# Performance work log

Measured on AMD Instinct MI355X. Metric: run time of the kernel, lower is better.

The kernel has to match this reference:

```python
import jax, jax.numpy as jnp
import numpy as np
import math

N_HEADS = 32
N_KV_HEADS = 8
HEAD_DIM = 64
ROPE_BASE = 10000.0


def _rope_cos_sin(L, dtype):
    # inv_freq: [head_dim/2]
    inv_freq = 1.0 / (ROPE_BASE ** (jnp.arange(0, HEAD_DIM, 2, dtype=jnp.float32) / HEAD_DIM))
    t = jnp.arange(L, dtype=jnp.float32)
    freqs = jnp.outer(t, inv_freq)            # [L, head_dim/2]
    emb = jnp.concatenate([freqs, freqs], -1)  # [L, head_dim]
    return jnp.cos(emb).astype(dtype), jnp.sin(emb).astype(dtype)


def _rotate_half(x):
    x1, x2 = jnp.split(x, 2, axis=-1)
    return jnp.concatenate([-x2, x1], axis=-1)


def setup_inputs() -> dict:
    key = jax.random.key(0)
    ks = jax.random.split(key, 5)
    B, L, D = 2, 2048, 2048
    s = 0.02
    return {
        "x": jax.random.normal(ks[0], (B, L, D), jnp.float32),
        "Wq": jax.random.normal(ks[1], (D, N_HEADS * HEAD_DIM), jnp.float32) * s,
        "Wk": jax.random.normal(ks[2], (D, N_KV_HEADS * HEAD_DIM), jnp.float32) * s,
        "Wv": jax.random.normal(ks[3], (D, N_KV_HEADS * HEAD_DIM), jnp.float32) * s,
        "Wo": jax.random.normal(ks[4], (N_HEADS * HEAD_DIM, D), jnp.float32) * s,
    }


def reference(x, Wq, Wk, Wv, Wo):
    B, L, D = x.shape
    G = N_HEADS // N_KV_HEADS
    # QKV projections -> [B, H, L, hd]
    q = (x @ Wq).reshape(B, L, N_HEADS, HEAD_DIM).transpose(0, 2, 1, 3)
    k = (x @ Wk).reshape(B, L, N_KV_HEADS, HEAD_DIM).transpose(0, 2, 1, 3)
    v = (x @ Wv).reshape(B, L, N_KV_HEADS, HEAD_DIM).transpose(0, 2, 1, 3)
    # RoPE
    cos, sin = _rope_cos_sin(L, x.dtype)  # [L, hd]
    cos = cos[None, None]
    sin = sin[None, None]
    q = q * cos + _rotate_half(q) * sin
    k = k * cos + _rotate_half(k) * sin
    # GQA expand kv heads (repeat_interleave along head dim)
    k = jnp.repeat(k, G, axis=1)
    v = jnp.repeat(v, G, axis=1)
    # Causal SDPA
    scale = 1.0 / math.sqrt(HEAD_DIM)
    scores = jnp.einsum('bhqd,bhkd->bhqk', q, k) * scale  # [B,H,L,L]
    causal = jnp.tril(jnp.ones((L, L), bool))
    scores = jnp.where(causal[None, None], scores, jnp.finfo(scores.dtype).min)
    probs = jax.nn.softmax(scores, axis=-1)
    out = jnp.einsum('bhqk,bhkd->bhqd', probs, v)  # [B,H,L,hd]
    out = out.transpose(0, 2, 1, 3).reshape(B, L, N_HEADS * HEAD_DIM)
    return out @ Wo
```

## Files before the change

kernel.cpp:

```cpp
#include <hip/hip_runtime.h>
#include <hip/hip_bf16.h>
#include <stdint.h>

typedef __bf16 bf16_t;
typedef bf16_t bf16x2 __attribute__((ext_vector_type(2)));
typedef bf16_t bf16x4 __attribute__((ext_vector_type(4)));
typedef bf16_t bf16x8 __attribute__((ext_vector_type(8)));
typedef float f32x4 __attribute__((ext_vector_type(4)));
typedef float f32x16 __attribute__((ext_vector_type(16)));

#define NH 32
#define NKV 8
#define HD 64
#define LSEQ 2048
#define DMODEL 2048
#define BATCH 2

#define QSCALE 0.18033688011112042f
#define FIXED_M 12.0f

__device__ __forceinline__ void gl_lds16(const void* g, void* l) {
  __builtin_amdgcn_global_load_lds(
      (__attribute__((address_space(1))) char*)(uintptr_t)g,
      (__attribute__((address_space(3))) char*)(uintptr_t)l, 16, 0, 0);
}

__device__ __forceinline__ unsigned pack2(float a, float b) {
  bf16x2 t;
  t[0] = (bf16_t)a;
  t[1] = (bf16_t)b;
  return __builtin_bit_cast(unsigned, t);
}


__global__ void cvt_x(const float4* __restrict__ s, bf16x4* __restrict__ d, int n4) {
  int i = blockIdx.x * blockDim.x + threadIdx.x;
  if (i >= n4) return;
  float4 v = s[i];
  bf16x4 o;
  o[0] = (bf16_t)v.x; o[1] = (bf16_t)v.y; o[2] = (bf16_t)v.z; o[3] = (bf16_t)v.w;
  d[i] = o;
}

__global__ void transpose_w(const float* __restrict__ W, bf16_t* __restrict__ WT,
                            int K, int N) {
  __shared__ float tile[32][33];
  int nb = blockIdx.x * 32, kb = blockIdx.y * 32;
  int tx = threadIdx.x, ty = threadIdx.y;
#pragma unroll
  for (int i = 0; i < 32; i += 8)
    tile[ty + i][tx] = W[(size_t)(kb + ty + i) * N + nb + tx];
  __syncthreads();
#pragma unroll
  for (int i = 0; i < 32; i += 8)
    WT[(size_t)(nb + ty + i) * K + kb + tx] = (bf16_t)tile[tx][ty + i];
}

__global__ void rope_table(float* __restrict__ cosT, float* __restrict__ sinT) {
  int t = blockIdx.x * blockDim.x + threadIdx.x;
  int l = t >> 5, i = t & 31;
  float inv = powf(10000.0f, -(float)i / 32.0f);
  float ang = (float)l * inv;
  float s, c;
  sincosf(ang, &s, &c);
  cosT[t] = c;
  sinT[t] = s;
}

template <int EPI, int NREP>
__global__ __launch_bounds__(512, 1) void gemm256(
    const bf16_t* __restrict__ A, const bf16_t* __restrict__ BT,
    float* __restrict__ Cf, bf16_t* __restrict__ Qo, bf16_t* __restrict__ Ko,
    bf16_t* __restrict__ Vo, int M, int N, int K,
    const float* __restrict__ cosT, const float* __restrict__ sinT, int nx) {
  constexpr int BN = NREP * 64;
  __shared__ bf16_t Al[2][4 * 4096];
  __shared__ bf16_t Bl[2][NREP * 4096];
  const int tid = threadIdx.x, lane = tid & 63, w = tid >> 6;
  const int wm = w >> 2, wn = w & 3;
  const int r15 = lane & 15, g = lane >> 4;
  const int nwg = (int)gridDim.x;
  const int sid = ((int)blockIdx.x & 7) * (nwg >> 3) + ((int)blockIdx.x >> 3);
  const int m0 = (sid / nx) * 256, n0 = (sid % nx) * BN;

  f32x4 acc[8][NREP] = {};

  const int NT = K >> 6;
  const int NI = NT >> 1;

  auto stage_q = [&](bf16_t* dst, const bf16_t* src, int row0, int kt) {
    const int r = tid >> 3;
    const int sc = (((tid & 7) ^ (r & 7)) << 3);
    gl_lds16(src + (size_t)(row0 + r) * K + (kt << 6) + sc, dst + tid * 8);
  };
  auto stage_step = [&](int d, int kt, int s) {
    kt = kt < NT ? kt : NT - 1;
    if (NREP == 4) {
      if (s == 0) { stage_q(&Bl[d][0], BT, n0, kt); stage_q(&Bl[d][4096], BT, n0 + 64, kt); }
      else if (s == 1) { stage_q(&Bl[d][8192], BT, n0 + 128, kt); stage_q(&Bl[d][12288], BT, n0 + 192, kt); }
      else if (s == 2) { stage_q(&Al[d][0], A, m0, kt); stage_q(&Al[d][8192], A, m0 + 128, kt); }
      else { stage_q(&Al[d][4096], A, m0 + 64, kt); stage_q(&Al[d][12288], A, m0 + 192, kt); }
    } else {
      if (s == 0) { stage_q(&Bl[d][0], BT, n0, kt); stage_q(&Bl[d][4096], BT, n0 + 64, kt); }
      else if (s == 1) { stage_q(&Al[d][0], A, m0, kt); stage_q(&Al[d][8192], A, m0 + 128, kt); }
      else if (s == 2) { stage_q(&Al[d][4096], A, m0 + 64, kt); stage_q(&Al[d][12288], A, m0 + 192, kt); }
    }
  };
  auto lda = [&](int d, int mi, int kk) -> bf16x8 {
    const int ar = (wm << 7) + (mi << 4) + r15;
    return *(const bf16x8*)((const char*)&Al[d][(ar >> 6) << 12] +
                            (ar & 63) * 128 + ((((kk << 2) + g) ^ (ar & 7)) << 4));
  };
  auto ldb = [&](int d, int ni, int kk) -> bf16x8 {
    const int br = wn * (NREP << 4) + (ni << 4) + r15;
    return *(const bf16x8*)((const char*)&Bl[d][(br >> 6) << 12] +
                            (br & 63) * 128 + ((((kk << 2) + g) ^ (br & 7)) << 4));
  };

  stage_step(0, 0, 0);
  stage_step(0, 0, 1);
  stage_step(0, 0, 2);
  stage_step(0, 0, 3);

  for (int i = 0; i < NI; ++i) {
#pragma unroll
    for (int hf = 0; hf < 2; ++hf) {
      const int dC = hf;
      const int dS = hf ^ 1;
      const int ktS = (i << 1) + 1 + hf;
      bf16x8 bf0[NREP][2];
#pragma unroll
      for (int q = 0; q < 4; ++q) {
        stage_step(dS, ktS, q);
        if (q == 0) asm volatile("s_waitcnt vmcnt(4)" ::: "memory");
        if (q == 2) asm volatile("s_waitcnt vmcnt(6)" ::: "memory");
        __builtin_amdgcn_s_barrier();
        asm volatile("" ::: "memory");
        if (q == 0) {
#pragma unroll
          for (int ni = 0; ni < NREP; ++ni)
#pragma unroll
            for (int kk = 0; kk < 2; ++kk) bf0[ni][kk] = ldb(dC, ni, kk);
        }
        bf16x8 af[2][2];
#pragma unroll
        for (int t2 = 0; t2 < 2; ++t2)
#pragma unroll
          for (int kk = 0; kk < 2; ++kk) af[t2][kk] = lda(dC, 2 * q + t2, kk);
        __builtin_amdgcn_s_setprio(1);
#pragma unroll
        for (int t2 = 0; t2 < 2; ++t2)
#pragma unroll
          for (int ni = 0; ni < NREP; ++ni)
#pragma unroll
            for (int kk = 0; kk < 2; ++kk)
              acc[2 * q + t2][ni] = __builtin_amdgcn_mfma_f32_16x16x32_bf16(
                  af[t2][kk], bf0[ni][kk], acc[2 * q + t2][ni], 0, 0, 0);
        __builtin_amdgcn_s_setprio(0);
        asm volatile("" ::: "memory");
        __builtin_amdgcn_s_barrier();
      }
    }
  }
  asm volatile("s_waitcnt vmcnt(0)" ::: "memory");

  if constexpr (EPI == 0) {
#pragma unroll
    for (int mi = 0; mi < 8; ++mi) {
      const int row = m0 + wm * 128 + mi * 16 + g * 4;
#pragma unroll
      for (int ni = 0; ni < NREP; ++ni) {
        const int col = n0 + wn * (NREP * 16) + ni * 16 + r15;
#pragma unroll
        for (int r = 0; r < 4; ++r)
          Cf[(size_t)(row + r) * N + col] = acc[mi][ni][r];
      }
    }
  } else {
    const int colbase = n0 + wn * 64;
    auto rope_store = [&](bf16_t* C, int NHT, int colrel, float sc) {
#pragma unroll
      for (int mi = 0; mi < 8; ++mi)
#pragma unroll
        for (int r = 0; r < 4; ++r) {
          const int rowg = m0 + wm * 128 + mi * 16 + g * 4 + r;
          const int bb = rowg >> 11, ls = rowg & (LSEQ - 1);
#pragma unroll
          for (int ni = 0; ni < 2; ++ni) {
            const int col = colrel + ni * 16 + r15;
            const int hh = col >> 6, d = col & 63;
            const float c = cosT[ls * 32 + d], s = sinT[ls * 32 + d];
            const float v0 = acc[mi][ni][r], v1 = acc[mi][ni + 2][r];
            bf16_t* dst = C + (((size_t)bb * NHT + hh) * LSEQ + ls) * HD + d;
            dst[0] = (bf16_t)((v0 * c - v1 * s) * sc);
            dst[32] = (bf16_t)((v1 * c + v0 * s) * sc);
          }
        }
    };
    if (n0 < 2048) {
      rope_store(Qo, NH, colbase, QSCALE);
    } else if (n0 < 2560) {
      rope_store(Ko, NKV, colbase - 2048, 1.0f);
    } else {
#pragma unroll
      for (int mi = 0; mi < 8; ++mi)
#pragma unroll
        for (int r = 0; r < 4; ++r) {
          const int rowg = m0 + wm * 128 + mi * 16 + g * 4 + r;
          const int bb = rowg >> 11, ls = rowg & (LSEQ - 1);
#pragma unroll
          for (int ni = 0; ni < 4; ++ni) {
            const int col = colbase - 2560 + ni * 16 + r15;
            const int hh = col >> 6, d = col & 63;
            Vo[(((size_t)bb * NKV + hh) * HD + d) * LSEQ + ls] =
                (bf16_t)acc[mi][ni][r];
          }
        }
    }
  }
}

__global__ __launch_bounds__(512, 4) void attn_fwd(
    const bf16_t* __restrict__ Q, const bf16_t* __restrict__ Kh,
    const bf16_t* __restrict__ VTh, bf16_t* __restrict__ AO) {
  __shared__ bf16_t Kl[2][64 * 64];
  __shared__ bf16_t Vl[2][64 * 64];
  const int tid = threadIdx.x, lane = tid & 63, w = tid >> 6;
  const int col = lane & 31, hi = lane >> 5;
  const int hk = (int)blockIdx.x & 7, b = (int)blockIdx.x >> 3;
  const int a = (int)blockIdx.y & 15, k = (int)blockIdx.y >> 4;
  const int qt = k ? 31 - a : a;
  const int h = hk * 4 + (w & 3);
  const int qoff = (w >> 2) * 32;

  const bf16_t* Qb =
      Q + (((size_t)b * NH + h) * LSEQ + (size_t)qt * 64 + qoff) * HD;
  const bf16_t* Kb = Kh + ((size_t)b * NKV + hk) * LSEQ * HD;
  const bf16_t* Vb = VTh + ((size_t)b * NKV + hk) * HD * LSEQ;

  const int nt = qt + 1;

  bf16x8 ones8;
#pragma unroll
  for (int j = 0; j < 8; ++j) ones8[j] = (bf16_t)1.0f;

  auto stage = [&](int buf, int kt) {
    const int row = tid >> 3, cc = tid & 7;
    const int scol = (cc ^ (row & 7)) * 16;
    gl_lds16((const char*)Kb + (size_t)(kt * 64 + row) * 128 + scol,
             (char*)&Kl[buf][0] + tid * 16);
    gl_lds16((const char*)Vb + (size_t)row * 4096 + (size_t)kt * 128 + scol,
             (char*)&Vl[buf][0] + tid * 16);
  };

  bf16x8 qf[4];
#pragma unroll
  for (int kc = 0; kc < 4; ++kc)
    qf[kc] = *(const bf16x8*)&Qb[(size_t)col * HD + kc * 16 + hi * 8];

  f32x16 o[2] = {};
  f32x16 osum = {};

  int cur = 0;
  stage(cur, 0);
  __syncthreads();
  for (int kt = 0; kt < nt; ++kt) {
    if (kt + 1 < nt) stage(cur ^ 1, kt + 1);
    const bool diag = (kt == nt - 1);
    const char* Kcur = (const char*)&Kl[cur][0];
    const char* Vcur = (const char*)&Vl[cur][0];

    f32x16 sfrag[2] = {};
#pragma unroll
    for (int kvs = 0; kvs < 2; ++kvs) {
      if (diag && kvs * 32 > 31 + qoff) {
#pragma unroll
        for (int r = 0; r < 16; ++r) sfrag[kvs][r] = -1e30f;
        continue;
      }
      bf16x8 ak[4];
#pragma unroll
      for (int kc = 0; kc < 4; ++kc) {
        const int row = kvs * 32 + col;
        const int slot = ((kc * 2 + hi) ^ (row & 7)) * 16;
        ak[kc] = *(const bf16x8*)(Kcur + row * 128 + slot);
      }
#pragma unroll
      for (int kc = 0; kc < 4; ++kc)
        sfrag[kvs] = __builtin_amdgcn_mfma_f32_32x32x16_bf16(
            ak[kc], qf[kc], sfrag[kvs], 0, 0, 0);
    }

    if (diag) {
#pragma unroll
      for (int kvs = 0; kvs < 2; ++kvs)
#pragma unroll
        for (int r = 0; r < 16; ++r) {
          const int kvl = kvs * 32 + (r & 3) + 8 * (r >> 2) + 4 * hi;
          if (kvl > col + qoff) sfrag[kvs][r] = -1e30f;
        }
    }

    bf16x8 pf[4];
#pragma unroll
    for (int kvs = 0; kvs < 2; ++kvs)
#pragma unroll
      for (int c1 = 0; c1 < 2; ++c1) {
        float pv[8];
#pragma unroll
        for (int j = 0; j < 8; ++j)
          pv[j] = __builtin_amdgcn_exp2f(sfrag[kvs][c1 * 8 + j] - FIXED_M);
        const unsigned a01 = pack2(pv[0], pv[1]), a23 = pack2(pv[2], pv[3]);
        const unsigned b01 = pack2(pv[4], pv[5]), b23 = pack2(pv[6], pv[7]);
        const unsigned s01 = __shfl_xor(hi ? a01 : b01, 32);
        const unsigned s23 = __shfl_xor(hi ? a23 : b23, 32);
        union { unsigned u[4]; bf16x8 v; } t;
        t.u[0] = hi ? s01 : a01;
        t.u[1] = hi ? s23 : a23;
        t.u[2] = hi ? b01 : s01;
        t.u[3] = hi ? b23 : s23;
        pf[kvs * 2 + c1] = t.v;
      }

#pragma unroll
    for (int ds = 0; ds < 2; ++ds) {
      bf16x8 av[4];
#pragma unroll
      for (int kc2 = 0; kc2 < 4; ++kc2) {
        const int row = ds * 32 + col;
        const int slot = ((kc2 * 2 + hi) ^ (row & 7)) * 16;
        av[kc2] = *(const bf16x8*)(Vcur + row * 128 + slot);
      }
#pragma unroll
      for (int kc2 = 0; kc2 < 4; ++kc2) {
        if (diag && kc2 * 16 > 31 + qoff) continue;
        o[ds] = __builtin_amdgcn_mfma_f32_32x32x16_bf16(
            av[kc2], pf[kc2], o[ds], 0, 0, 0);
      }
    }
#pragma unroll
    for (int kc2 = 0; kc2 < 4; ++kc2) {
      if (diag && kc2 * 16 > 31 + qoff) continue;
      osum = __builtin_amdgcn_mfma_f32_32x32x16_bf16(
          ones8, pf[kc2], osum, 0, 0, 0);
    }

    __syncthreads();
    cur ^= 1;
  }

  const float inv = 1.0f / osum[0];
  const int q = qt * 64 + qoff + col;
#pragma unroll
  for (int ds = 0; ds < 2; ++ds)
#pragma unroll
    for (int g4 = 0; g4 < 4; ++g4) {
      bf16x4 o4;
#pragma unroll
      for (int j = 0; j < 4; ++j) o4[j] = (bf16_t)(o[ds][g4 * 4 + j] * inv);
      const int d = ds * 32 + 8 * g4 + 4 * hi;
      *(bf16x4*)&AO[((size_t)b * LSEQ + q) * DMODEL + h * HD + d] = o4;
    }
}


extern "C" void kernel_launch(void* const* d_in, const int* in_sizes, int n_in,
                              void* d_out, int out_size, void* d_ws, size_t ws_size,
                              hipStream_t stream) {
  const float* x = (const float*)d_in[0];
  const float* Wq = (const float*)d_in[1];
  const float* Wk = (const float*)d_in[2];
  const float* Wv = (const float*)d_in[3];
  const float* Wo = (const float*)d_in[4];
  char* ws = (char*)d_ws;
  size_t off = 0;
  auto alloc = [&](size_t bytes) {
    char* p = ws + off;
    off += (bytes + 255) & ~(size_t)255;
    return p;
  };
  bf16_t* xb = (bf16_t*)alloc((size_t)BATCH * LSEQ * DMODEL * 2);
  bf16_t* wqkvT = (bf16_t*)alloc((size_t)3072 * DMODEL * 2);
  bf16_t* wot = (bf16_t*)alloc((size_t)DMODEL * DMODEL * 2);
  float* cosT = (float*)alloc((size_t)LSEQ * 32 * 4);
  float* sinT = (float*)alloc((size_t)LSEQ * 32 * 4);
  bf16_t* Qh = (bf16_t*)alloc((size_t)BATCH * NH * LSEQ * HD * 2);
  bf16_t* Kh = (bf16_t*)alloc((size_t)BATCH * NKV * LSEQ * HD * 2);
  bf16_t* VTh = (bf16_t*)alloc((size_t)BATCH * NKV * HD * LSEQ * 2);
  bf16_t* AO = (bf16_t*)alloc((size_t)BATCH * LSEQ * NH * HD * 2);
  (void)ws_size; (void)in_sizes; (void)n_in; (void)out_size;

  const int M = BATCH * LSEQ;

  cvt_x<<<(M * DMODEL / 4 + 255) / 256, 256, 0, stream>>>(
      (const float4*)x, (bf16x4*)xb, M * DMODEL / 4);
  transpose_w<<<dim3(64, 64), dim3(32, 8), 0, stream>>>(Wq, wqkvT, 2048, 2048);
  transpose_w<<<dim3(16, 64), dim3(32, 8), 0, stream>>>(
      Wk, wqkvT + (size_t)2048 * 2048, 2048, 512);
  transpose_w<<<dim3(16, 64), dim3(32, 8), 0, stream>>>(
      Wv, wqkvT + (size_t)2560 * 2048, 2048, 512);
  transpose_w<<<dim3(64, 64), dim3(32, 8), 0, stream>>>(Wo, wot, 2048, 2048);
  rope_table<<<LSEQ * 32 / 256, 256, 0, stream>>>(cosT, sinT);

  gemm256<3, 4><<<192, 512, 0, stream>>>(
      xb, wqkvT, nullptr, Qh, Kh, VTh, M, 3072, 2048, cosT, sinT, 12);

  attn_fwd<<<dim3(16, 32), 512, 0, stream>>>(Qh, Kh, VTh, AO);

  gemm256<0, 2><<<256, 512, 0, stream>>>(
      AO, wot, (float*)d_out, nullptr, nullptr, nullptr, M, 2048, 2048,
      nullptr, nullptr, 16);
}
```

Baseline: 173.8 us.

## Replace pipelined 256x256 QKV GEMM with simple 128x128 tile kernel

The QKV projection moves from a 256x256-tile, 512-thread, double-buffered LDS-pipelined GEMM (192 blocks) to a new 128x128-tile, 256-thread kernel with a single LDS buffer and plain syncthreads (768 blocks, up to 3 per CU). The aim is a better fit of work to the CU count and more occupancy to hide latency. In exchange it gives up the explicit load/compute overlap and accepts more global traffic from the smaller tiles. The output-projection GEMM is kept, with its unused epilogue parameters removed.

Result: no change. 173.3 us (-0.3%).

```diff
diff --git a/kernel.cpp b/kernel.cpp
--- a/kernel.cpp
+++ b/kernel.cpp
@@ -67,110 +67,64 @@
   sinT[t] = s;
 }
 
-template <int EPI, int NREP>
-__global__ __launch_bounds__(512, 1) void gemm256(
+template <int EPI>
+__global__ __launch_bounds__(256, 3) void gemm128(
     const bf16_t* __restrict__ A, const bf16_t* __restrict__ BT,
     float* __restrict__ Cf, bf16_t* __restrict__ Qo, bf16_t* __restrict__ Ko,
     bf16_t* __restrict__ Vo, int M, int N, int K,
     const float* __restrict__ cosT, const float* __restrict__ sinT, int nx) {
-  constexpr int BN = NREP * 64;
-  __shared__ bf16_t Al[2][4 * 4096];
-  __shared__ bf16_t Bl[2][NREP * 4096];
+  __shared__ bf16_t Al[128 * 64];
+  __shared__ bf16_t Bl[128 * 64];
   const int tid = threadIdx.x, lane = tid & 63, w = tid >> 6;
-  const int wm = w >> 2, wn = w & 3;
+  const int wm = w >> 1, wn = w & 1;
   const int r15 = lane & 15, g = lane >> 4;
   const int nwg = (int)gridDim.x;
   const int sid = ((int)blockIdx.x & 7) * (nwg >> 3) + ((int)blockIdx.x >> 3);
-  const int m0 = (sid / nx) * 256, n0 = (sid % nx) * BN;
-
-  f32x4 acc[8][NREP] = {};
-
-  const int NT = K >> 6;
-  const int NI = NT >> 1;
-
-  auto stage_q = [&](bf16_t* dst, const bf16_t* src, int row0, int kt) {
-    const int r = tid >> 3;
-    const int sc = (((tid & 7) ^ (r & 7)) << 3);
-    gl_lds16(src + (size_t)(row0 + r) * K + (kt << 6) + sc, dst + tid * 8);
-  };
-  auto stage_step = [&](int d, int kt, int s) {
-    kt = kt < NT ? kt : NT - 1;
-    if (NREP == 4) {
-      if (s == 0) { stage_q(&Bl[d][0], BT, n0, kt); stage_q(&Bl[d][4096], BT, n0 + 64, kt); }
-      else if (s == 1) { stage_q(&Bl[d][8192], BT, n0 + 128, kt); stage_q(&Bl[d][12288], BT, n0 + 192, kt); }
-      else if (s == 2) { stage_q(&Al[d][0], A, m0, kt); stage_q(&Al[d][8192], A, m0 + 128, kt); }
-      else { stage_q(&Al[d][4096], A, m0 + 64, kt); stage_q(&Al[d][12288], A, m0 + 192, kt); }
-    } else {
-      if (s == 0) { stage_q(&Bl[d][0], BT, n0, kt); stage_q(&Bl[d][4096], BT, n0 + 64, kt); }
-      else if (s == 1) { stage_q(&Al[d][0], A, m0, kt); stage_q(&Al[d][8192], A, m0 + 128, kt); }
-      else if (s == 2) { stage_q(&Al[d][4096], A, m0 + 64, kt); stage_q(&Al[d][12288], A, m0 + 192, kt); }
-    }
-  };
-  auto lda = [&](int d, int mi, int kk) -> bf16x8 {
-    const int ar = (wm << 7) + (mi << 4) + r15;
-    return *(const bf16x8*)((const char*)&Al[d][(ar >> 6) << 12] +
-                            (ar & 63) * 128 + ((((kk << 2) + g) ^ (ar & 7)) << 4));
-  };
-  auto ldb = [&](int d, int ni, int kk) -> bf16x8 {
-    const int br = wn * (NREP << 4) + (ni << 4) + r15;
-    return *(const bf16x8*)((const char*)&Bl[d][(br >> 6) << 12] +
-                            (br & 63) * 128 + ((((kk << 2) + g) ^ (br & 7)) << 4));
-  };
-
-  stage_step(0, 0, 0);
-  stage_step(0, 0, 1);
-  stage_step(0, 0, 2);
-  stage_step(0, 0, 3);
-
-  for (int i = 0; i < NI; ++i) {
-#pragma unroll
-    for (int hf = 0; hf < 2; ++hf) {
-      const int dC = hf;
-      const int dS = hf ^ 1;
-      const int ktS = (i << 1) + 1 + hf;
-      bf16x8 bf0[NREP][2];
-#pragma unroll
-      for (int q = 0; q < 4; ++q) {
-        stage_step(dS, ktS, q);
-        if (q == 0) asm volatile("s_waitcnt vmcnt(4)" ::: "memory");
-        if (q == 2) asm volatile("s_waitcnt vmcnt(6)" ::: "memory");
-        __builtin_amdgcn_s_barrier();
-        asm volatile("" ::: "memory");
-        if (q == 0) {
-#pragma unroll
-          for (int ni = 0; ni < NREP; ++ni)
-#pragma unroll
-            for (int kk = 0; kk < 2; ++kk) bf0[ni][kk] = ldb(dC, ni, kk);
-        }
-        bf16x8 af[2][2];
-#pragma unroll
-        for (int t2 = 0; t2 < 2; ++t2)
-#pragma unroll
-          for (int kk = 0; kk < 2; ++kk) af[t2][kk] = lda(dC, 2 * q + t2, kk);
-        __builtin_amdgcn_s_setprio(1);
-#pragma unroll
-        for (int t2 = 0; t2 < 2; ++t2)
-#pragma unroll
-          for (int ni = 0; ni < NREP; ++ni)
-#pragma unroll
-            for (int kk = 0; kk < 2; ++kk)
-              acc[2 * q + t2][ni] = __builtin_amdgcn_mfma_f32_16x16x32_bf16(
-                  af[t2][kk], bf0[ni][kk], acc[2 * q + t2][ni], 0, 0, 0);
-        __builtin_amdgcn_s_setprio(0);
-        asm volatile("" ::: "memory");
-        __builtin_amdgcn_s_barrier();
-      }
-    }
+  const int m0 = (sid / nx) * 128, n0 = (sid % nx) * 128;
+  f32x4 acc[4][4] = {};
+
+  for (int kt = 0; kt < K; kt += 64) {
+#pragma unroll
+    for (int i = 0; i < 4; ++i) {
+      const int c = i * 256 + tid;
+      const int row = c >> 3, cc = c & 7;
+      const int sc = (cc ^ (row & 7)) * 8;
+      gl_lds16(A + (size_t)(m0 + row) * K + kt + sc, Al + c * 8);
+      gl_lds16(BT + (size_t)(n0 + row) * K + kt + sc, Bl + c * 8);
+    }
+    __syncthreads();
+#pragma unroll
+    for (int kk = 0; kk < 2; ++kk) {
+      bf16x8 af[4], bfr[4];
+#pragma unroll
+      for (int mi = 0; mi < 4; ++mi) {
+        const int r = wm * 64 + mi * 16 + r15;
+        af[mi] = *(const bf16x8*)((const char*)Al + r * 128 +
+                                  (((kk * 4 + g) ^ (r & 7)) << 4));
+      }
+#pragma unroll
+      for (int ni = 0; ni < 4; ++ni) {
+        const int r = wn * 64 + ni * 16 + r15;
+        bfr[ni] = *(const bf16x8*)((const char*)Bl + r * 128 +
+                                   (((kk * 4 + g) ^ (r & 7)) << 4));
+      }
+#pragma unroll
+      for (int mi = 0; mi < 4; ++mi)
+#pragma unroll
+        for (int ni = 0; ni < 4; ++ni)
+          acc[mi][ni] = __builtin_amdgcn_mfma_f32_16x16x32_bf16(
+              af[mi], bfr[ni], acc[mi][ni], 0, 0, 0);
+    }
+    __syncthreads();
   }
-  asm volatile("s_waitcnt vmcnt(0)" ::: "memory");
 
   if constexpr (EPI == 0) {
 #pragma unroll
-    for (int mi = 0; mi < 8; ++mi) {
-      const int row = m0 + wm * 128 + mi * 16 + g * 4;
-#pragma unroll
-      for (int ni = 0; ni < NREP; ++ni) {
-        const int col = n0 + wn * (NREP * 16) + ni * 16 + r15;
+    for (int mi = 0; mi < 4; ++mi) {
+      const int row = m0 + wm * 64 + mi * 16 + g * 4;
+#pragma unroll
+      for (int ni = 0; ni < 4; ++ni) {
+        const int col = n0 + wn * 64 + ni * 16 + r15;
 #pragma unroll
         for (int r = 0; r < 4; ++r)
           Cf[(size_t)(row + r) * N + col] = acc[mi][ni][r];
@@ -180,10 +134,10 @@
     const int colbase = n0 + wn * 64;
     auto rope_store = [&](bf16_t* C, int NHT, int colrel, float sc) {
 #pragma unroll
-      for (int mi = 0; mi < 8; ++mi)
+      for (int mi = 0; mi < 4; ++mi)
 #pragma unroll
         for (int r = 0; r < 4; ++r) {
-          const int rowg = m0 + wm * 128 + mi * 16 + g * 4 + r;
+          const int rowg = m0 + wm * 64 + mi * 16 + g * 4 + r;
           const int bb = rowg >> 11, ls = rowg & (LSEQ - 1);
 #pragma unroll
           for (int ni = 0; ni < 2; ++ni) {
@@ -203,10 +157,10 @@
       rope_store(Ko, NKV, colbase - 2048, 1.0f);
     } else {
 #pragma unroll
-      for (int mi = 0; mi < 8; ++mi)
+      for (int mi = 0; mi < 4; ++mi)
 #pragma unroll
         for (int r = 0; r < 4; ++r) {
-          const int rowg = m0 + wm * 128 + mi * 16 + g * 4 + r;
+          const int rowg = m0 + wm * 64 + mi * 16 + g * 4 + r;
           const int bb = rowg >> 11, ls = rowg & (LSEQ - 1);
 #pragma unroll
           for (int ni = 0; ni < 4; ++ni) {
@@ -216,6 +170,106 @@
                 (bf16_t)acc[mi][ni][r];
           }
         }
+    }
+  }
+}
+
+template <int EPI, int NREP>
+__global__ __launch_bounds__(512, 1) void gemm256(
+    const bf16_t* __restrict__ A, const bf16_t* __restrict__ BT,
+    float* __restrict__ Cf, int M, int N, int K, int nx) {
+  __shared__ bf16_t Al[2][4 * 4096];
+  __shared__ bf16_t Bl[2][NREP * 4096];
+  const int tid = threadIdx.x, lane = tid & 63, w = tid >> 6;
+  const int wm = w >> 2, wn = w & 3;
+  const int r15 = lane & 15, g = lane >> 4;
+  const int nwg = (int)gridDim.x;
+  const int sid = ((int)blockIdx.x & 7) * (nwg >> 3) + ((int)blockIdx.x >> 3);
+  const int m0 = (sid / nx) * 256, n0 = (sid % nx) * (NREP * 64);
+
+  f32x4 acc[8][NREP] = {};
+
+  const int NT = K >> 6;
+  const int NI = NT >> 1;
+
+  auto stage_q = [&](bf16_t* dst, const bf16_t* src, int row0, int kt) {
+    const int r = tid >> 3;
+    const int sc = (((tid & 7) ^ (r & 7)) << 3);
+    gl_lds16(src + (size_t)(row0 + r) * K + (kt << 6) + sc, dst + tid * 8);
+  };
+  auto stage_step = [&](int d, int kt, int s) {
+    kt = kt < NT ? kt : NT - 1;
+    if (s == 0) { stage_q(&Bl[d][0], BT, n0, kt); stage_q(&Bl[d][4096], BT, n0 + 64, kt); }
+    else if (s == 1) { stage_q(&Al[d][0], A, m0, kt); stage_q(&Al[d][8192], A, m0 + 128, kt); }
+    else if (s == 2) { stage_q(&Al[d][4096], A, m0 + 64, kt); stage_q(&Al[d][12288], A, m0 + 192, kt); }
+  };
+  auto lda = [&](int d, int mi, int kk) -> bf16x8 {
+    const int ar = (wm << 7) + (mi << 4) + r15;
+    return *(const bf16x8*)((const char*)&Al[d][(ar >> 6) << 12] +
+                            (ar & 63) * 128 + ((((kk << 2) + g) ^ (ar & 7)) << 4));
+  };
+  auto ldb = [&](int d, int ni, int kk) -> bf16x8 {
+    const int br = wn * (NREP << 4) + (ni << 4) + r15;
+    return *(const bf16x8*)((const char*)&Bl[d][(br >> 6) << 12] +
+                            (br & 63) * 128 + ((((kk << 2) + g) ^ (br & 7)) << 4));
+  };
+
+  stage_step(0, 0, 0);
+  stage_step(0, 0, 1);
+  stage_step(0, 0, 2);
+  stage_step(0, 0, 3);
+
+  for (int i = 0; i < NI; ++i) {
+#pragma unroll
+    for (int hf = 0; hf < 2; ++hf) {
+      const int dC = hf;
+      const int dS = hf ^ 1;
+      const int ktS = (i << 1) + 1 + hf;
+      bf16x8 bf0[NREP][2];
+#pragma unroll
+      for (int q = 0; q < 4; ++q) {
+        stage_step(dS, ktS, q);
+        if (q == 0) asm volatile("s_waitcnt vmcnt(4)" ::: "memory");
+        if (q == 2) asm volatile("s_waitcnt vmcnt(6)" ::: "memory");
+        __builtin_amdgcn_s_barrier();
+        asm volatile("" ::: "memory");
+        if (q == 0) {
+#pragma unroll
+          for (int ni = 0; ni < NREP; ++ni)
+#pragma unroll
+            for (int kk = 0; kk < 2; ++kk) bf0[ni][kk] = ldb(dC, ni, kk);
+        }
+        bf16x8 af[2][2];
+#pragma unroll
+        for (int t2 = 0; t2 < 2; ++t2)
+#pragma unroll
+          for (int kk = 0; kk < 2; ++kk) af[t2][kk] = lda(dC, 2 * q + t2, kk);
+        __builtin_amdgcn_s_setprio(1);
+#pragma unroll
+        for (int t2 = 0; t2 < 2; ++t2)
+#pragma unroll
+          for (int ni = 0; ni < NREP; ++ni)
+#pragma unroll
+            for (int kk = 0; kk < 2; ++kk)
+              acc[2 * q + t2][ni] = __builtin_amdgcn_mfma_f32_16x16x32_bf16(
+                  af[t2][kk], bf0[ni][kk], acc[2 * q + t2][ni], 0, 0, 0);
+        __builtin_amdgcn_s_setprio(0);
+        asm volatile("" ::: "memory");
+        __builtin_amdgcn_s_barrier();
+      }
+    }
+  }
+  asm volatile("s_waitcnt vmcnt(0)" ::: "memory");
+
+#pragma unroll
+  for (int mi = 0; mi < 8; ++mi) {
+    const int row = m0 + wm * 128 + mi * 16 + g * 4;
+#pragma unroll
+    for (int ni = 0; ni < NREP; ++ni) {
+      const int col = n0 + wn * (NREP * 16) + ni * 16 + r15;
+#pragma unroll
+      for (int r = 0; r < 4; ++r)
+        Cf[(size_t)(row + r) * N + col] = acc[mi][ni][r];
     }
   }
 }
@@ -402,12 +456,11 @@
   transpose_w<<<dim3(64, 64), dim3(32, 8), 0, stream>>>(Wo, wot, 2048, 2048);
   rope_table<<<LSEQ * 32 / 256, 256, 0, stream>>>(cosT, sinT);
 
-  gemm256<3, 4><<<192, 512, 0, stream>>>(
-      xb, wqkvT, nullptr, Qh, Kh, VTh, M, 3072, 2048, cosT, sinT, 12);
+  gemm128<3><<<768, 256, 0, stream>>>(
+      xb, wqkvT, nullptr, Qh, Kh, VTh, M, 3072, 2048, cosT, sinT, 24);
 
   attn_fwd<<<dim3(16, 32), 512, 0, stream>>>(Qh, Kh, VTh, AO);
 
   gemm256<0, 2><<<256, 512, 0, stream>>>(
-      AO, wot, (float*)d_out, nullptr, nullptr, nullptr, M, 2048, 2048,
-      nullptr, nullptr, 16);
-}
+      AO, wot, (float*)d_out, M, 2048, 2048, 16);
+}
```

## Shrink QKV GEMM tile to 256x192 and interleave RoPE pairs in weights

Applied to the files above, without the earlier changes.

Changes the fused QKV projection GEMM from 256x256 tiles (192 blocks) to 256x192 tiles (256 blocks), so the grid fills the device more evenly. A 192-wide tile no longer lines up with 64-wide heads, so the Wq/Wk rows are permuted during transpose to interleave each rotate-half pair (d, d+32) into adjacent columns. RoPE is then applied per 16-column fragment using a lane shuffle. Each block reuses A less per tile in exchange for better occupancy, and the staging schedule becomes uneven.

After: 194.6 us. +12.0%, slower.

```diff
diff --git a/kernel.cpp b/kernel.cpp
--- a/kernel.cpp
+++ b/kernel.cpp
@@ -42,6 +42,7 @@
   d[i] = o;
 }
 
+template <bool PERM>
 __global__ void transpose_w(const float* __restrict__ W, bf16_t* __restrict__ WT,
                             int K, int N) {
   __shared__ float tile[32][33];
@@ -52,8 +53,14 @@
     tile[ty + i][tx] = W[(size_t)(kb + ty + i) * N + nb + tx];
   __syncthreads();
 #pragma unroll
-  for (int i = 0; i < 32; i += 8)
-    WT[(size_t)(nb + ty + i) * K + kb + tx] = (bf16_t)tile[tx][ty + i];
+  for (int i = 0; i < 32; i += 8) {
+    int r = nb + ty + i;
+    if (PERM) {
+      const int d = r & 63;
+      r = (r & ~63) | (d < 32 ? 2 * d : 2 * (d - 32) + 1);
+    }
+    WT[(size_t)r * K + kb + tx] = (bf16_t)tile[tx][ty + i];
+  }
 }
 
 __global__ void rope_table(float* __restrict__ cosT, float* __restrict__ sinT) {
@@ -73,7 +80,6 @@
     float* __restrict__ Cf, bf16_t* __restrict__ Qo, bf16_t* __restrict__ Ko,
     bf16_t* __restrict__ Vo, int M, int N, int K,
     const float* __restrict__ cosT, const float* __restrict__ sinT, int nx) {
-  constexpr int BN = NREP * 64;
   __shared__ bf16_t Al[2][4 * 4096];
   __shared__ bf16_t Bl[2][NREP * 4096];
   const int tid = threadIdx.x, lane = tid & 63, w = tid >> 6;
@@ -81,7 +87,7 @@
   const int r15 = lane & 15, g = lane >> 4;
   const int nwg = (int)gridDim.x;
   const int sid = ((int)blockIdx.x & 7) * (nwg >> 3) + ((int)blockIdx.x >> 3);
-  const int m0 = (sid / nx) * 256, n0 = (sid % nx) * BN;
+  const int m0 = (sid / nx) * 256, n0 = (sid % nx) * (NREP * 64);
 
   f32x4 acc[8][NREP] = {};
 
@@ -95,11 +101,11 @@
   };
   auto stage_step = [&](int d, int kt, int s) {
     kt = kt < NT ? kt : NT - 1;
-    if (NREP == 4) {
+    if constexpr (NREP == 3) {
       if (s == 0) { stage_q(&Bl[d][0], BT, n0, kt); stage_q(&Bl[d][4096], BT, n0 + 64, kt); }
-      else if (s == 1) { stage_q(&Bl[d][8192], BT, n0 + 128, kt); stage_q(&Bl[d][12288], BT, n0 + 192, kt); }
-      else if (s == 2) { stage_q(&Al[d][0], A, m0, kt); stage_q(&Al[d][8192], A, m0 + 128, kt); }
-      else { stage_q(&Al[d][4096], A, m0 + 64, kt); stage_q(&Al[d][12288], A, m0 + 192, kt); }
+      else if (s == 1) { stage_q(&Bl[d][8192], BT, n0 + 128, kt); stage_q(&Al[d][0], A, m0, kt); }
+      else if (s == 2) { stage_q(&Al[d][8192], A, m0 + 128, kt); stage_q(&Al[d][4096], A, m0 + 64, kt); }
+      else { stage_q(&Al[d][12288], A, m0 + 192, kt); }
     } else {
       if (s == 0) { stage_q(&Bl[d][0], BT, n0, kt); stage_q(&Bl[d][4096], BT, n0 + 64, kt); }
       else if (s == 1) { stage_q(&Al[d][0], A, m0, kt); stage_q(&Al[d][8192], A, m0 + 128, kt); }
@@ -177,45 +183,45 @@
       }
     }
   } else {
-    const int colbase = n0 + wn * 64;
-    auto rope_store = [&](bf16_t* C, int NHT, int colrel, float sc) {
+    const int colbase = n0 + wn * 48;
+    auto rope_store_ni = [&](bf16_t* C, int NHT, int colrel16, float sc, int ni) {
 #pragma unroll
       for (int mi = 0; mi < 8; ++mi)
 #pragma unroll
         for (int r = 0; r < 4; ++r) {
           const int rowg = m0 + wm * 128 + mi * 16 + g * 4 + r;
           const int bb = rowg >> 11, ls = rowg & (LSEQ - 1);
-#pragma unroll
-          for (int ni = 0; ni < 2; ++ni) {
-            const int col = colrel + ni * 16 + r15;
-            const int hh = col >> 6, d = col & 63;
-            const float c = cosT[ls * 32 + d], s = sinT[ls * 32 + d];
-            const float v0 = acc[mi][ni][r], v1 = acc[mi][ni + 2][r];
-            bf16_t* dst = C + (((size_t)bb * NHT + hh) * LSEQ + ls) * HD + d;
-            dst[0] = (bf16_t)((v0 * c - v1 * s) * sc);
-            dst[32] = (bf16_t)((v1 * c + v0 * s) * sc);
-          }
+          const int col = colrel16 + r15;
+          const int hh = col >> 6;
+          const int p = (col & 63) >> 1;
+          const float c = cosT[ls * 32 + p], s = sinT[ls * 32 + p];
+          const float v = acc[mi][ni][r];
+          const float vp = __shfl_xor(v, 1);
+          const float out = (r15 & 1) ? (v * c + vp * s) : (v * c - vp * s);
+          const int d = p + ((r15 & 1) << 5);
+          C[(((size_t)bb * NHT + hh) * LSEQ + ls) * HD + d] = (bf16_t)(out * sc);
         }
     };
-    if (n0 < 2048) {
-      rope_store(Qo, NH, colbase, QSCALE);
-    } else if (n0 < 2560) {
-      rope_store(Ko, NKV, colbase - 2048, 1.0f);
-    } else {
-#pragma unroll
-      for (int mi = 0; mi < 8; ++mi)
-#pragma unroll
-        for (int r = 0; r < 4; ++r) {
-          const int rowg = m0 + wm * 128 + mi * 16 + g * 4 + r;
-          const int bb = rowg >> 11, ls = rowg & (LSEQ - 1);
-#pragma unroll
-          for (int ni = 0; ni < 4; ++ni) {
-            const int col = colbase - 2560 + ni * 16 + r15;
+#pragma unroll
+    for (int ni = 0; ni < NREP; ++ni) {
+      const int col16 = colbase + ni * 16;
+      if (col16 < 2048) {
+        rope_store_ni(Qo, NH, col16, QSCALE, ni);
+      } else if (col16 < 2560) {
+        rope_store_ni(Ko, NKV, col16 - 2048, 1.0f, ni);
+      } else {
+#pragma unroll
+        for (int mi = 0; mi < 8; ++mi)
+#pragma unroll
+          for (int r = 0; r < 4; ++r) {
+            const int rowg = m0 + wm * 128 + mi * 16 + g * 4 + r;
+            const int bb = rowg >> 11, ls = rowg & (LSEQ - 1);
+            const int col = col16 - 2560 + r15;
             const int hh = col >> 6, d = col & 63;
             Vo[(((size_t)bb * NKV + hh) * HD + d) * LSEQ + ls] =
                 (bf16_t)acc[mi][ni][r];
           }
-        }
+      }
     }
   }
 }
@@ -394,16 +400,16 @@
 
   cvt_x<<<(M * DMODEL / 4 + 255) / 256, 256, 0, stream>>>(
       (const float4*)x, (bf16x4*)xb, M * DMODEL / 4);
-  transpose_w<<<dim3(64, 64), dim3(32, 8), 0, stream>>>(Wq, wqkvT, 2048, 2048);
-  transpose_w<<<dim3(16, 64), dim3(32, 8), 0, stream>>>(
+  transpose_w<true><<<dim3(64, 64), dim3(32, 8), 0, stream>>>(Wq, wqkvT, 2048, 2048);
+  transpose_w<true><<<dim3(16, 64), dim3(32, 8), 0, stream>>>(
       Wk, wqkvT + (size_t)2048 * 2048, 2048, 512);
-  transpose_w<<<dim3(16, 64), dim3(32, 8), 0, stream>>>(
+  transpose_w<false><<<dim3(16, 64), dim3(32, 8), 0, stream>>>(
       Wv, wqkvT + (size_t)2560 * 2048, 2048, 512);
-  transpose_w<<<dim3(64, 64), dim3(32, 8), 0, stream>>>(Wo, wot, 2048, 2048);
+  transpose_w<false><<<dim3(64, 64), dim3(32, 8), 0, stream>>>(Wo, wot, 2048, 2048);
   rope_table<<<LSEQ * 32 / 256, 256, 0, stream>>>(cosT, sinT);
 
-  gemm256<3, 4><<<192, 512, 0, stream>>>(
-      xb, wqkvT, nullptr, Qh, Kh, VTh, M, 3072, 2048, cosT, sinT, 12);
+  gemm256<4, 3><<<256, 512, 0, stream>>>(
+      xb, wqkvT, nullptr, Qh, Kh, VTh, M, 3072, 2048, cosT, sinT, 16);
 
   attn_fwd<<<dim3(16, 32), 512, 0, stream>>>(Qh, Kh, VTh, AO);
 
```
